# Performance work log

Hardware: AMD Instinct MI355X
Metric: run time of the kernel (lower is better)

Reference implementation:

```python
import jax, jax.numpy as jnp
import numpy as np

BS, QLEN, DIM, NH = 2, 2048, 1024, 16
HD = DIM // NH


def setup_inputs() -> dict:
    key = jax.random.key(0)
    ks = jax.random.split(key, 6)
    std = 0.02
    return {
        "x": jax.random.normal(ks[0], (BS, QLEN, DIM), dtype=jnp.float32),
        "mask": jnp.ones((BS, QLEN), dtype=jnp.float32),
        "Wq": jax.random.normal(ks[1], (DIM, DIM), dtype=jnp.float32) * std,
        "bq": jnp.zeros((DIM,), dtype=jnp.float32),
        "Wk": jax.random.normal(ks[2], (DIM, DIM), dtype=jnp.float32) * std,
        "bk": jnp.zeros((DIM,), dtype=jnp.float32),
        "Wv": jax.random.normal(ks[3], (DIM, DIM), dtype=jnp.float32) * std,
        "bv": jnp.zeros((DIM,), dtype=jnp.float32),
        "Wo": jax.random.normal(ks[4], (DIM, DIM), dtype=jnp.float32) * std,
        "bo": jnp.zeros((DIM,), dtype=jnp.float32),
    }


def reference(x, mask, Wq, bq, Wk, bk, Wv, bv, Wo, bo):
    bs, qlen, dim = x.shape
    # project and split heads: [bs, nh, len, hd]
    def split_heads(t):
        return t.reshape(bs, -1, NH, HD).transpose(0, 2, 1, 3)

    q = split_heads(x @ Wq + bq) / jnp.sqrt(jnp.float32(HD))
    k = split_heads(x @ Wk + bk)
    v = split_heads(x @ Wv + bv)

    scores = jnp.einsum("bhqd,bhkd->bhqk", q, k)  # [bs, nh, qlen, klen]
    m = mask.reshape(bs, 1, 1, -1)  # 2D mask -> broadcast over heads and q
    scores = scores - 1e30 * (1.0 - m)
    weights = jax.nn.softmax(scores, axis=-1)
    # dropout p=0.0 at inference -> no-op; head_mask is None
    context = jnp.einsum("bhqk,bhkd->bhqd", weights, v)
    context = context.transpose(0, 2, 1, 3).reshape(bs, qlen, NH * HD)
    return context @ Wo + bo
```

## Files before the change

kernel.cpp:

```cpp
#include <hip/hip_runtime.h>
#include <stdint.h>

#define BSZ  2
#define SEQ  2048
#define DIM  1024
#define NHD  16
#define HD   64
#define MTOT (BSZ*SEQ)

using short8  = __attribute__((ext_vector_type(8))) short;
using floatx4 = __attribute__((ext_vector_type(4))) float;

#define QSCALE 0.18033688011112042f
#define BIGM   1.44e30f

__device__ __forceinline__ unsigned short f2bf(float f) {
    unsigned int u = __float_as_uint(f);
    u += 0x7fffu + ((u >> 16) & 1u);
    return (unsigned short)(u >> 16);
}
__device__ __forceinline__ unsigned int pk2r(float a, float b) {
    unsigned int ua = __float_as_uint(a) + 0x8000u;
    unsigned int ub = __float_as_uint(b) + 0x8000u;
    return __builtin_amdgcn_perm(ub, ua, 0x07060302);
}
__device__ __forceinline__ unsigned int cvtpk(float a, float b) {
    unsigned int r;
    asm("v_cvt_pk_bf16_f32 %0, %1, %2" : "=v"(r) : "v"(a), "v"(b));
    return r;
}

__device__ __forceinline__ void gll16(const void* g, const void* lds) {
    unsigned int loff = (unsigned int)(unsigned long long)lds;
    __builtin_amdgcn_global_load_lds(
        (const __attribute__((address_space(1))) unsigned int*)g,
        (__attribute__((address_space(3))) unsigned int*)loff, 16, 0, 0);
}

__global__ __launch_bounds__(256)
void conv_x(const float* __restrict__ X, const float* __restrict__ mask,
            unsigned short* __restrict__ Xbf, float* __restrict__ Pen) {
    size_t i = ((size_t)blockIdx.x * 256 + threadIdx.x) * 8;
    float4 a = *(const float4*)(X + i);
    float4 b = *(const float4*)(X + i + 4);
    uint4 u = {pk2r(a.x, a.y), pk2r(a.z, a.w), pk2r(b.x, b.y), pk2r(b.z, b.w)};
    *(uint4*)(Xbf + i) = u;
    if (blockIdx.x < 2) {
        const size_t j = ((size_t)blockIdx.x * 256 + threadIdx.x) * 8;
        float4 m0 = *(const float4*)(mask + j);
        float4 m1 = *(const float4*)(mask + j + 4);
        float4 r0 = {__builtin_fmaf(m0.x, BIGM, -BIGM), __builtin_fmaf(m0.y, BIGM, -BIGM),
                     __builtin_fmaf(m0.z, BIGM, -BIGM), __builtin_fmaf(m0.w, BIGM, -BIGM)};
        float4 r1 = {__builtin_fmaf(m1.x, BIGM, -BIGM), __builtin_fmaf(m1.y, BIGM, -BIGM),
                     __builtin_fmaf(m1.z, BIGM, -BIGM), __builtin_fmaf(m1.w, BIGM, -BIGM)};
        *(float4*)(Pen + j)     = r0;
        *(float4*)(Pen + j + 4) = r1;
    }
}

__global__ __launch_bounds__(256)
void conv_wt(const float* __restrict__ Wq, const float* __restrict__ Wk,
             const float* __restrict__ Wv, const float* __restrict__ Wo,
             unsigned short* __restrict__ Wt3, unsigned short* __restrict__ Wto)
{
    __shared__ float tile[64 * 65];
    const int z = blockIdx.z;
    const float* W = (z == 0) ? Wq : (z == 1) ? Wk : (z == 2) ? Wv : Wo;
    unsigned short* out = (z < 3) ? (Wt3 + (size_t)z * DIM * DIM) : Wto;
    const int k0 = blockIdx.x * 64, n0 = blockIdx.y * 64;
    const int t = threadIdx.x;
    const int r = t >> 2, c0 = (t & 3) * 16;
#pragma unroll
    for (int j = 0; j < 4; ++j) {
        float4 v = *(const float4*)&W[(size_t)(k0 + r) * DIM + n0 + c0 + j * 4];
        tile[r * 65 + c0 + j * 4 + 0] = v.x;
        tile[r * 65 + c0 + j * 4 + 1] = v.y;
        tile[r * 65 + c0 + j * 4 + 2] = v.z;
        tile[r * 65 + c0 + j * 4 + 3] = v.w;
    }
    __syncthreads();
    unsigned int p[8];
#pragma unroll
    for (int j = 0; j < 8; ++j)
        p[j] = pk2r(tile[(c0 + 2 * j) * 65 + r], tile[(c0 + 2 * j + 1) * 65 + r]);
    uint4 u0 = {p[0], p[1], p[2], p[3]}, u1 = {p[4], p[5], p[6], p[7]};
    unsigned short* dst = out + (size_t)(n0 + r) * DIM + k0 + c0;
    *(uint4*)dst = u0;
    *(uint4*)(dst + 8) = u1;
}

__global__ __launch_bounds__(256)
void qkv_gemm(const unsigned short* __restrict__ Xbf,
              const unsigned short* __restrict__ Wt3,
              const float* __restrict__ bq, const float* __restrict__ bk,
              const float* __restrict__ bv,
              unsigned short* __restrict__ Qb,
              unsigned short* __restrict__ Kb,
              unsigned short* __restrict__ VbT)
{
    __shared__ unsigned short As[2][128 * 32];
    __shared__ unsigned short Bs[2][128 * 32];

    const int t = threadIdx.x, w = t >> 6, lane = t & 63;
    const int lm = lane & 15, grp = lane >> 4;
    const int wm = w >> 1, wn = w & 1;
    const int m0 = blockIdx.x * 128;
    const int mat = blockIdx.y >> 3;
    const int n0 = (blockIdx.y & 7) * 128;
    const unsigned short* Bg = Wt3 + (size_t)mat * DIM * DIM;
    const int lr = lane >> 2, lc = (lane & 3) * 8;
    const int r0 = w * 16;
    const bool swap = (mat != 2);

    const unsigned short* xs0 = Xbf + (size_t)(m0 + r0 + lr) * DIM + lc;
    const unsigned short* xs1 = Xbf + (size_t)(m0 + 64 + r0 + lr) * DIM + lc;
    const unsigned short* ws0 = Bg  + (size_t)(n0 + r0 + lr) * DIM + lc;
    const unsigned short* ws1 = Bg  + (size_t)(n0 + 64 + r0 + lr) * DIM + lc;

    const unsigned short* afb[2];
    const unsigned short* bfb[2];
#pragma unroll
    for (int u = 0; u < 2; ++u) {
        afb[u] = &As[u][(wm * 64 + lm) * 32 + grp * 8];
        bfb[u] = &Bs[u][(wn * 64 + lm) * 32 + grp * 8];
    }

    floatx4 acc[4][4];
#pragma unroll
    for (int i = 0; i < 4; ++i)
#pragma unroll
        for (int j = 0; j < 4; ++j) acc[i][j] = (floatx4){0.f, 0.f, 0.f, 0.f};

#define QKV_STAGE(BUF) do {                                    \
        gll16(xs0, &As[BUF][r0 * 32]);                         \
        gll16(xs1, &As[BUF][(64 + r0) * 32]);                  \
        gll16(ws0, &Bs[BUF][r0 * 32]);                         \
        gll16(ws1, &Bs[BUF][(64 + r0) * 32]);                  \
        xs0 += 32; xs1 += 32; ws0 += 32; ws1 += 32;            \
    } while (0)

#define QKV_BODY(CUR) do {                                                    \
        __syncthreads();                                                      \
        QKV_STAGE(CUR ^ 1);                                                   \
        short8 af[4], bf[4];                                                  \
        _Pragma("unroll")                                                     \
        for (int mt = 0; mt < 4; ++mt)                                        \
            af[mt] = *(const short8*)(afb[CUR] + mt * 512);                   \
        _Pragma("unroll")                                                     \
        for (int nt = 0; nt < 4; ++nt)                                        \
            bf[nt] = *(const short8*)(bfb[CUR] + nt * 512);                   \
        if (swap) {                                                           \
            _Pragma("unroll")                                                 \
            for (int mt = 0; mt < 4; ++mt)                                    \
                _Pragma("unroll")                                             \
                for (int nt = 0; nt < 4; ++nt)                                \
                    acc[mt][nt] = __builtin_amdgcn_mfma_f32_16x16x32_bf16(    \
                        bf[nt], af[mt], acc[mt][nt], 0, 0, 0);                \
        } else {                                                              \
            _Pragma("unroll")                                                 \
            for (int mt = 0; mt < 4; ++mt)                                    \
                _Pragma("unroll")                                             \
                for (int nt = 0; nt < 4; ++nt)                                \
                    acc[mt][nt] = __builtin_amdgcn_mfma_f32_16x16x32_bf16(    \
                        af[mt], bf[nt], acc[mt][nt], 0, 0, 0);                \
        }                                                                     \
    } while (0)

    QKV_STAGE(0);
#pragma unroll 1
    for (int it = 0; it < DIM / 64; ++it) {
        QKV_BODY(0);
        QKV_BODY(1);
    }
#undef QKV_BODY
#undef QKV_STAGE

    if (mat == 2) {
#pragma unroll
        for (int nt = 0; nt < 4; ++nt) {
            const int c = n0 + wn * 64 + nt * 16 + lm;
            const float bb = bv[c];
            const int h = c >> 6, d = c & 63;
#pragma unroll
            for (int mt = 0; mt < 4; ++mt) {
                const int r = m0 + wm * 64 + mt * 16 + grp * 4;
                const int b = r >> 11, s = r & 2047;
                const int si = s & 63, sb = s & ~63;
                const int cg = si >> 4, g = (si >> 2) & 3;
                const int unit = (((cg & 1) << 2) | g) ^ (d & 7);
                const int sph = sb + unit * 8 + ((cg >> 1) << 2);
                uint2 pv;
                pv.x = pk2r(acc[mt][nt][0] + bb, acc[mt][nt][1] + bb);
                pv.y = pk2r(acc[mt][nt][2] + bb, acc[mt][nt][3] + bb);
                *(uint2*)&VbT[(((size_t)(b * NHD + h)) * HD + d) * SEQ + sph] = pv;
            }
        }
    } else {
        const float* bias = (mat == 0) ? bq : bk;
        unsigned short* dst = (mat == 0) ? Qb : Kb;
        const float sc = (mat == 0) ? QSCALE : 1.0f;
#pragma unroll
        for (int nt = 0; nt < 4; ++nt) {
            const int c0 = n0 + wn * 64 + nt * 16 + grp * 4;
            float4 bb = *(const float4*)&bias[c0];
            const int h = c0 >> 6, d0 = c0 & 63;
#pragma unroll
            for (int mt = 0; mt < 4; ++mt) {
                const int r = m0 + wm * 64 + mt * 16 + lm;
                const int b = r >> 11, s = r & 2047;
                uint2 pv;
                pv.x = pk2r((acc[mt][nt][0] + bb.x) * sc, (acc[mt][nt][1] + bb.y) * sc);
                pv.y = pk2r((acc[mt][nt][2] + bb.z) * sc, (acc[mt][nt][3] + bb.w) * sc);
                const int dd = (mat == 0) ? d0
                             : ((((d0 >> 3) ^ (s & 7)) << 3) | (d0 & 7));
                *(uint2*)&dst[(((size_t)(b * NHD + h)) * SEQ + s) * HD + dd] = pv;
            }
        }
    }
}

__global__ __launch_bounds__(256, 4)
void attn(const unsigned short* __restrict__ Qb,
          const unsigned short* __restrict__ Kb,
          const unsigned short* __restrict__ VbT,
          const float* __restrict__ Pen,
          unsigned short* __restrict__ Cb)
{
    __shared__ unsigned short Kt[2][64 * 64];
    __shared__ unsigned short Vt[2][64 * 64];

    const int t = threadIdx.x, w = t >> 6, lane = t & 63;
    const int lm = lane & 15, grp = lane >> 4;
    const int x7 = lm & 7;

    const int lin = blockIdx.y * (int)gridDim.x + blockIdx.x;
    const int swz = (lin & 7) * ((SEQ / 64) * (BSZ * NHD) / 8) + (lin >> 3);
    const int bh = swz >> 5, b = bh >> 4, h = bh & 15;
    const int q0 = (swz & 31) * 64;

    short8 qf[2];
    {
        const unsigned short* qrow = Qb + ((size_t)bh * SEQ + q0 + w * 16 + lm) * HD;
        qf[0] = *(const short8*)(qrow + grp * 8);
        qf[1] = *(const short8*)(qrow + 32 + grp * 8);
    }

    const unsigned int one2 = 0x3f803f80u;
    uint4 onesu = {one2, one2, one2, one2};
    short8 ones = *(const short8*)&onesu;

    floatx4 oacc[4];
#pragma unroll
    for (int i = 0; i < 4; ++i) oacc[i] = (floatx4){0.f, 0.f, 0.f, 0.f};
    floatx4 lacc = (floatx4){0.f, 0.f, 0.f, 0.f};

    const unsigned short* Kg = Kb + (size_t)bh * SEQ * HD;
    const unsigned short* Vg = VbT + (size_t)bh * HD * SEQ;
    const int srow = lane >> 3, scol = (lane & 7) * 8;

    const unsigned short* kp0 = Kg + (size_t)(w * 16 + srow) * HD + scol;
    const unsigned short* kp1 = kp0 + 8 * HD;
    const unsigned short* vp0 = Vg + (size_t)(w * 16 + srow) * SEQ + scol;
    const unsigned short* vp1 = vp0 + 8 * SEQ;

    gll16(kp0, &Kt[0][(w * 16) * 64]);
    gll16(kp1, &Kt[0][(w * 16 + 8) * 64]);
    gll16(vp0, &Vt[0][(w * 16) * 64]);
    gll16(vp1, &Vt[0][(w * 16 + 8) * 64]);
    kp0 += 64 * HD; kp1 += 64 * HD; vp0 += 64; vp1 += 64;

    const unsigned short* kba[2]; const unsigned short* kbb[2];
    const unsigned short* vba[2]; const unsigned short* vbb[2];
#pragma unroll
    for (int u = 0; u < 2; ++u) {
        kba[u] = &Kt[u][lm * 64 + ((grp    ) ^ x7) * 8];
        kbb[u] = &Kt[u][lm * 64 + ((4 + grp) ^ x7) * 8];
        vba[u] = &Vt[u][lm * 64 + ((grp    ) ^ x7) * 8];
        vbb[u] = &Vt[u][lm * 64 + ((4 + grp) ^ x7) * 8];
    }
    const float* mp = Pen + (size_t)b * SEQ + grp * 4;

#define ATTN_BODY(CUR) do {                                                   \
        __syncthreads();                                                      \
        gll16(kp0, &Kt[CUR ^ 1][(w * 16) * 64]);                              \
        gll16(kp1, &Kt[CUR ^ 1][(w * 16 + 8) * 64]);                          \
        gll16(vp0, &Vt[CUR ^ 1][(w * 16) * 64]);                              \
        gll16(vp1, &Vt[CUR ^ 1][(w * 16 + 8) * 64]);                          \
        kp0 += 64 * HD; kp1 += 64 * HD; vp0 += 64; vp1 += 64;                 \
        float4 mdv[4];                                                        \
        _Pragma("unroll")                                                     \
        for (int cg = 0; cg < 4; ++cg)                                        \
            mdv[cg] = *(const float4*)(mp + cg * 16);                         \
        mp += 64;                                                             \
        floatx4 sv[4];                                                        \
        __builtin_amdgcn_s_setprio(1);                                        \
        _Pragma("unroll")                                                     \
        for (int cg = 0; cg < 4; ++cg) {                                      \
            short8 a0 = *(const short8*)(kba[CUR] + cg * 1024);               \
            short8 a1 = *(const short8*)(kbb[CUR] + cg * 1024);               \
            floatx4 s = (floatx4){mdv[cg].x, mdv[cg].y, mdv[cg].z, mdv[cg].w}; \
            s = __builtin_amdgcn_mfma_f32_16x16x32_bf16(a0, qf[0], s, 0, 0, 0); \
            s = __builtin_amdgcn_mfma_f32_16x16x32_bf16(a1, qf[1], s, 0, 0, 0); \
            sv[cg] = s;                                                       \
        }                                                                     \
        __builtin_amdgcn_s_setprio(0);                                        \
        short8 vf[4][2];                                                      \
        _Pragma("unroll")                                                     \
        for (int dg = 0; dg < 4; ++dg) {                                      \
            vf[dg][0] = *(const short8*)(vba[CUR] + dg * 1024);               \
            vf[dg][1] = *(const short8*)(vbb[CUR] + dg * 1024);               \
        }                                                                     \
        float p[4][4];                                                        \
        _Pragma("unroll")                                                     \
        for (int cg = 0; cg < 4; ++cg) {                                      \
            p[cg][0] = __builtin_exp2f(sv[cg][0]);                            \
            p[cg][1] = __builtin_exp2f(sv[cg][1]);                            \
            p[cg][2] = __builtin_exp2f(sv[cg][2]);                            \
            p[cg][3] = __builtin_exp2f(sv[cg][3]);                            \
        }                                                                     \
        uint4 u0, u1;                                                         \
        u0.x = cvtpk(p[0][0], p[0][1]); u0.y = cvtpk(p[0][2], p[0][3]);       \
        u0.z = cvtpk(p[2][0], p[2][1]); u0.w = cvtpk(p[2][2], p[2][3]);       \
        u1.x = cvtpk(p[1][0], p[1][1]); u1.y = cvtpk(p[1][2], p[1][3]);       \
        u1.z = cvtpk(p[3][0], p[3][1]); u1.w = cvtpk(p[3][2], p[3][3]);       \
        short8 ap0 = *(const short8*)&u0;                                     \
        short8 ap1 = *(const short8*)&u1;                                     \
        __builtin_amdgcn_s_setprio(1);                                        \
        _Pragma("unroll")                                                     \
        for (int dg = 0; dg < 4; ++dg) {                                      \
            oacc[dg] = __builtin_amdgcn_mfma_f32_16x16x32_bf16(ap0, vf[dg][0], oacc[dg], 0, 0, 0); \
            oacc[dg] = __builtin_amdgcn_mfma_f32_16x16x32_bf16(ap1, vf[dg][1], oacc[dg], 0, 0, 0); \
        }                                                                     \
        lacc = __builtin_amdgcn_mfma_f32_16x16x32_bf16(ap0, ones, lacc, 0, 0, 0); \
        lacc = __builtin_amdgcn_mfma_f32_16x16x32_bf16(ap1, ones, lacc, 0, 0, 0); \
        __builtin_amdgcn_s_setprio(0);                                        \
    } while (0)

#pragma unroll 1
    for (int it = 0; it < SEQ / 128; ++it) {
        ATTN_BODY(0);
        ATTN_BODY(1);
    }
#undef ATTN_BODY

    float inv[4];
#pragma unroll
    for (int r = 0; r < 4; ++r) inv[r] = (lacc[r] > 0.f) ? 1.0f / lacc[r] : 0.f;
#pragma unroll
    for (int dg = 0; dg < 4; ++dg)
#pragma unroll
        for (int r = 0; r < 4; ++r) {
            const int s = q0 + w * 16 + grp * 4 + r;
            Cb[((size_t)(b * SEQ + s)) * DIM + h * HD + dg * 16 + lm] =
                f2bf(oacc[dg][r] * inv[r]);
        }
}

__global__ __launch_bounds__(256)
void out_gemm(const unsigned short* __restrict__ Cb,
              const unsigned short* __restrict__ Wto,
              const float* __restrict__ bo,
              float* __restrict__ out)
{
    __shared__ unsigned short As[2][128 * 32];
    __shared__ unsigned short Bs[2][64 * 32];

    const int t = threadIdx.x, w = t >> 6, lane = t & 63;
    const int lm = lane & 15, grp = lane >> 4;
    const int m0 = blockIdx.x * 128;
    const int n0 = blockIdx.y * 64;
    const int lr = lane >> 2, lc = (lane & 3) * 8;
    const int r0 = w * 16;

    const unsigned short* cs0 = Cb  + (size_t)(m0 + r0 + lr) * DIM + lc;
    const unsigned short* cs1 = Cb  + (size_t)(m0 + 64 + r0 + lr) * DIM + lc;
    const unsigned short* ws0 = Wto + (size_t)(n0 + r0 + lr) * DIM + lc;

    const unsigned short* afb[2];
    const unsigned short* bfb[2];
#pragma unroll
    for (int u = 0; u < 2; ++u) {
        afb[u] = &As[u][(w * 32 + lm) * 32 + grp * 8];
        bfb[u] = &Bs[u][lm * 32 + grp * 8];
    }

    floatx4 acc[2][4];
#pragma unroll
    for (int i = 0; i < 2; ++i)
#pragma unroll
        for (int j = 0; j < 4; ++j) acc[i][j] = (floatx4){0.f, 0.f, 0.f, 0.f};

#define OUT_STAGE(BUF) do {                                    \
        gll16(cs0, &As[BUF][r0 * 32]);                         \
        gll16(cs1, &As[BUF][(64 + r0) * 32]);                  \
        gll16(ws0, &Bs[BUF][r0 * 32]);                         \
        cs0 += 32; cs1 += 32; ws0 += 32;                       \
    } while (0)

#define OUT_BODY(CUR) do {                                                    \
        __syncthreads();                                                      \
        OUT_STAGE(CUR ^ 1);                                                   \
        short8 af[2], bf[4];                                                  \
        _Pragma("unroll")                                                     \
        for (int mt = 0; mt < 2; ++mt)                                        \
            af[mt] = *(const short8*)(afb[CUR] + mt * 512);                   \
        _Pragma("unroll")                                                     \
        for (int nt = 0; nt < 4; ++nt)                                        \
            bf[nt] = *(const short8*)(bfb[CUR] + nt * 512);                   \
        _Pragma("unroll")                                                     \
        for (int mt = 0; mt < 2; ++mt)                                        \
            _Pragma("unroll")                                                 \
            for (int nt = 0; nt < 4; ++nt)                                    \
                acc[mt][nt] = __builtin_amdgcn_mfma_f32_16x16x32_bf16(        \
                    bf[nt], af[mt], acc[mt][nt], 0, 0, 0);                    \
    } while (0)

    OUT_STAGE(0);
#pragma unroll 1
    for (int it = 0; it < DIM / 64; ++it) {
        OUT_BODY(0);
        OUT_BODY(1);
    }
#undef OUT_BODY
#undef OUT_STAGE

#pragma unroll
    for (int nt = 0; nt < 4; ++nt) {
        const int c0 = n0 + nt * 16 + grp * 4;
        float4 bb = *(const float4*)&bo[c0];
#pragma unroll
        for (int mt = 0; mt < 2; ++mt) {
            const int r = m0 + w * 32 + mt * 16 + lm;
            float4 o = {acc[mt][nt][0] + bb.x, acc[mt][nt][1] + bb.y,
                        acc[mt][nt][2] + bb.z, acc[mt][nt][3] + bb.w};
            *(float4*)&out[(size_t)r * DIM + c0] = o;
        }
    }
}

extern "C" void kernel_launch(void* const* d_in, const int* in_sizes, int n_in,
                              void* d_out, int out_size, void* d_ws, size_t ws_size,
                              hipStream_t stream)
{
    const float* x    = (const float*)d_in[0];
    const float* mask = (const float*)d_in[1];
    const float* Wq   = (const float*)d_in[2];
    const float* bq   = (const float*)d_in[3];
    const float* Wk   = (const float*)d_in[4];
    const float* bk   = (const float*)d_in[5];
    const float* Wv   = (const float*)d_in[6];
    const float* bv   = (const float*)d_in[7];
    const float* Wo   = (const float*)d_in[8];
    const float* bo   = (const float*)d_in[9];
    float* out = (float*)d_out;

    const size_t M1 = (size_t)DIM * DIM;
    unsigned short* Qb  = (unsigned short*)d_ws;
    unsigned short* Kb  = Qb  + 4 * M1;
    unsigned short* VbT = Kb  + 4 * M1;
    unsigned short* Cb  = VbT + 4 * M1;
    unsigned short* Xbf = Cb  + 4 * M1;
    unsigned short* Wt3 = Xbf + 4 * M1;
    unsigned short* Wto = Wt3 + 3 * M1;
    float*          Pen = (float*)(Wto + M1);

    conv_x <<<dim3((MTOT * DIM) / 2048), 256, 0, stream>>>(x, mask, Xbf, Pen);
    conv_wt<<<dim3(16, 16, 4), 256, 0, stream>>>(Wq, Wk, Wv, Wo, Wt3, Wto);
    qkv_gemm<<<dim3(MTOT / 128, 24), 256, 0, stream>>>(Xbf, Wt3, bq, bk, bv, Qb, Kb, VbT);
    attn<<<dim3(SEQ / 64, BSZ * NHD), 256, 0, stream>>>(Qb, Kb, VbT, Pen, Cb);
    out_gemm<<<dim3(MTOT / 128, DIM / 64), 256, 0, stream>>>(Cb, Wto, bo, out);
}
```

Before: 201.7 us.

## Give each attention wave two query tiles and stage mask in LDS

The attention kernel drops to 128 threads per block, and each wave now handles 32 query rows (two 16-row groups) instead of 16. Each K/V fragment read from LDS therefore feeds twice as many MFMAs, which reduces LDS traffic per unit of work. The per-batch mask penalty vector is loaded once into shared memory rather than read from global memory on every iteration. In exchange, register pressure rises, launch bounds change, fewer waves per block share each barrier, and LDS use per block grows by 8KB.

```diff
diff --git a/kernel.cpp b/kernel.cpp
--- a/kernel.cpp
+++ b/kernel.cpp
@@ -219,7 +219,7 @@
     }
 }
 
-__global__ __launch_bounds__(256, 4)
+__global__ __launch_bounds__(128, 2)
 void attn(const unsigned short* __restrict__ Qb,
           const unsigned short* __restrict__ Kb,
           const unsigned short* __restrict__ VbT,
@@ -228,6 +228,7 @@
 {
     __shared__ unsigned short Kt[2][64 * 64];
     __shared__ unsigned short Vt[2][64 * 64];
+    __shared__ float Msk[SEQ];
 
     const int t = threadIdx.x, w = t >> 6, lane = t & 63;
     const int lm = lane & 15, grp = lane >> 4;
@@ -238,36 +239,51 @@
     const int bh = swz >> 5, b = bh >> 4, h = bh & 15;
     const int q0 = (swz & 31) * 64;
 
-    short8 qf[2];
-    {
-        const unsigned short* qrow = Qb + ((size_t)bh * SEQ + q0 + w * 16 + lm) * HD;
-        qf[0] = *(const short8*)(qrow + grp * 8);
-        qf[1] = *(const short8*)(qrow + 32 + grp * 8);
+    short8 qf[2][2];
+#pragma unroll
+    for (int g = 0; g < 2; ++g) {
+        const unsigned short* qrow =
+            Qb + ((size_t)bh * SEQ + q0 + w * 32 + g * 16 + lm) * HD;
+        qf[g][0] = *(const short8*)(qrow + grp * 8);
+        qf[g][1] = *(const short8*)(qrow + 32 + grp * 8);
     }
 
     const unsigned int one2 = 0x3f803f80u;
     uint4 onesu = {one2, one2, one2, one2};
-    short8 ones = *(const short8*)&onesu;
-
-    floatx4 oacc[4];
-#pragma unroll
-    for (int i = 0; i < 4; ++i) oacc[i] = (floatx4){0.f, 0.f, 0.f, 0.f};
-    floatx4 lacc = (floatx4){0.f, 0.f, 0.f, 0.f};
+    const short8 ones = *(const short8*)&onesu;
+
+    floatx4 oacc[2][4];
+#pragma unroll
+    for (int g = 0; g < 2; ++g)
+#pragma unroll
+        for (int i = 0; i < 4; ++i) oacc[g][i] = (floatx4){0.f, 0.f, 0.f, 0.f};
+    floatx4 lacc0 = (floatx4){0.f, 0.f, 0.f, 0.f};
+    floatx4 lacc1 = (floatx4){0.f, 0.f, 0.f, 0.f};
 
     const unsigned short* Kg = Kb + (size_t)bh * SEQ * HD;
     const unsigned short* Vg = VbT + (size_t)bh * HD * SEQ;
     const int srow = lane >> 3, scol = (lane & 7) * 8;
 
-    const unsigned short* kp0 = Kg + (size_t)(w * 16 + srow) * HD + scol;
-    const unsigned short* kp1 = kp0 + 8 * HD;
-    const unsigned short* vp0 = Vg + (size_t)(w * 16 + srow) * SEQ + scol;
-    const unsigned short* vp1 = vp0 + 8 * SEQ;
-
-    gll16(kp0, &Kt[0][(w * 16) * 64]);
-    gll16(kp1, &Kt[0][(w * 16 + 8) * 64]);
-    gll16(vp0, &Vt[0][(w * 16) * 64]);
-    gll16(vp1, &Vt[0][(w * 16 + 8) * 64]);
-    kp0 += 64 * HD; kp1 += 64 * HD; vp0 += 64; vp1 += 64;
+    {
+        const float* pb = Pen + (size_t)b * SEQ;
+#pragma unroll
+        for (int j = 0; j < 4; ++j)
+            gll16(pb + (w * 4 + j) * 256 + lane * 4, &Msk[(w * 4 + j) * 256]);
+    }
+
+    const unsigned short* kp[4];
+    const unsigned short* vp[4];
+#pragma unroll
+    for (int j = 0; j < 4; ++j) {
+        kp[j] = Kg + (size_t)(w * 32 + j * 8 + srow) * HD + scol;
+        vp[j] = Vg + (size_t)(w * 32 + j * 8 + srow) * SEQ + scol;
+    }
+#pragma unroll
+    for (int j = 0; j < 4; ++j) {
+        gll16(kp[j], &Kt[0][(w * 32 + j * 8) * 64]);
+        gll16(vp[j], &Vt[0][(w * 32 + j * 8) * 64]);
+        kp[j] += 64 * HD; vp[j] += 64;
+    }
 
     const unsigned short* kba[2]; const unsigned short* kbb[2];
     const unsigned short* vba[2]; const unsigned short* vbb[2];
@@ -278,30 +294,32 @@
         vba[u] = &Vt[u][lm * 64 + ((grp    ) ^ x7) * 8];
         vbb[u] = &Vt[u][lm * 64 + ((4 + grp) ^ x7) * 8];
     }
-    const float* mp = Pen + (size_t)b * SEQ + grp * 4;
+    const float* mp = &Msk[grp * 4];
 
 #define ATTN_BODY(CUR) do {                                                   \
         __syncthreads();                                                      \
-        gll16(kp0, &Kt[CUR ^ 1][(w * 16) * 64]);                              \
-        gll16(kp1, &Kt[CUR ^ 1][(w * 16 + 8) * 64]);                          \
-        gll16(vp0, &Vt[CUR ^ 1][(w * 16) * 64]);                              \
-        gll16(vp1, &Vt[CUR ^ 1][(w * 16 + 8) * 64]);                          \
-        kp0 += 64 * HD; kp1 += 64 * HD; vp0 += 64; vp1 += 64;                 \
+        _Pragma("unroll")                                                     \
+        for (int j = 0; j < 4; ++j) {                                         \
+            gll16(kp[j], &Kt[CUR ^ 1][(w * 32 + j * 8) * 64]);                \
+            gll16(vp[j], &Vt[CUR ^ 1][(w * 32 + j * 8) * 64]);                \
+            kp[j] += 64 * HD; vp[j] += 64;                                    \
+        }                                                                     \
         float4 mdv[4];                                                        \
         _Pragma("unroll")                                                     \
         for (int cg = 0; cg < 4; ++cg)                                        \
             mdv[cg] = *(const float4*)(mp + cg * 16);                         \
         mp += 64;                                                             \
-        floatx4 sv[4];                                                        \
+        floatx4 sv0[4], sv1[4];                                               \
         __builtin_amdgcn_s_setprio(1);                                        \
         _Pragma("unroll")                                                     \
         for (int cg = 0; cg < 4; ++cg) {                                      \
             short8 a0 = *(const short8*)(kba[CUR] + cg * 1024);               \
             short8 a1 = *(const short8*)(kbb[CUR] + cg * 1024);               \
-            floatx4 s = (floatx4){mdv[cg].x, mdv[cg].y, mdv[cg].z, mdv[cg].w}; \
-            s = __builtin_amdgcn_mfma_f32_16x16x32_bf16(a0, qf[0], s, 0, 0, 0); \
-            s = __builtin_amdgcn_mfma_f32_16x16x32_bf16(a1, qf[1], s, 0, 0, 0); \
-            sv[cg] = s;                                                       \
+            floatx4 c0 = (floatx4){mdv[cg].x, mdv[cg].y, mdv[cg].z, mdv[cg].w}; \
+            floatx4 t0 = __builtin_amdgcn_mfma_f32_16x16x32_bf16(a0, qf[0][0], c0, 0, 0, 0); \
+            sv0[cg]    = __builtin_amdgcn_mfma_f32_16x16x32_bf16(a1, qf[0][1], t0, 0, 0, 0); \
+            floatx4 t1 = __builtin_amdgcn_mfma_f32_16x16x32_bf16(a0, qf[1][0], c0, 0, 0, 0); \
+            sv1[cg]    = __builtin_amdgcn_mfma_f32_16x16x32_bf16(a1, qf[1][1], t1, 0, 0, 0); \
         }                                                                     \
         __builtin_amdgcn_s_setprio(0);                                        \
         short8 vf[4][2];                                                      \
@@ -310,29 +328,43 @@
             vf[dg][0] = *(const short8*)(vba[CUR] + dg * 1024);               \
             vf[dg][1] = *(const short8*)(vbb[CUR] + dg * 1024);               \
         }                                                                     \
-        float p[4][4];                                                        \
+        float p0[4][4], p1[4][4];                                             \
         _Pragma("unroll")                                                     \
         for (int cg = 0; cg < 4; ++cg) {                                      \
-            p[cg][0] = __builtin_exp2f(sv[cg][0]);                            \
-            p[cg][1] = __builtin_exp2f(sv[cg][1]);                            \
-            p[cg][2] = __builtin_exp2f(sv[cg][2]);                            \
-            p[cg][3] = __builtin_exp2f(sv[cg][3]);                            \
+            p0[cg][0] = __builtin_exp2f(sv0[cg][0]);                          \
+            p0[cg][1] = __builtin_exp2f(sv0[cg][1]);                          \
+            p0[cg][2] = __builtin_exp2f(sv0[cg][2]);                          \
+            p0[cg][3] = __builtin_exp2f(sv0[cg][3]);                          \
+            p1[cg][0] = __builtin_exp2f(sv1[cg][0]);                          \
+            p1[cg][1] = __builtin_exp2f(sv1[cg][1]);                          \
+            p1[cg][2] = __builtin_exp2f(sv1[cg][2]);                          \
+            p1[cg][3] = __builtin_exp2f(sv1[cg][3]);                          \
         }                                                                     \
-        uint4 u0, u1;                                                         \
-        u0.x = cvtpk(p[0][0], p[0][1]); u0.y = cvtpk(p[0][2], p[0][3]);       \
-        u0.z = cvtpk(p[2][0], p[2][1]); u0.w = cvtpk(p[2][2], p[2][3]);       \
-        u1.x = cvtpk(p[1][0], p[1][1]); u1.y = cvtpk(p[1][2], p[1][3]);       \
-        u1.z = cvtpk(p[3][0], p[3][1]); u1.w = cvtpk(p[3][2], p[3][3]);       \
-        short8 ap0 = *(const short8*)&u0;                                     \
-        short8 ap1 = *(const short8*)&u1;                                     \
+        uint4 pu0, pu1, pu2, pu3;                                             \
+        pu0.x = cvtpk(p0[0][0], p0[0][1]); pu0.y = cvtpk(p0[0][2], p0[0][3]); \
+        pu0.z = cvtpk(p0[2][0], p0[2][1]); pu0.w = cvtpk(p0[2][2], p0[2][3]); \
+        pu1.x = cvtpk(p0[1][0], p0[1][1]); pu1.y = cvtpk(p0[1][2], p0[1][3]); \
+        pu1.z = cvtpk(p0[3][0], p0[3][1]); pu1.w = cvtpk(p0[3][2], p0[3][3]); \
+        pu2.x = cvtpk(p1[0][0], p1[0][1]); pu2.y = cvtpk(p1[0][2], p1[0][3]); \
+        pu2.z = cvtpk(p1[2][0], p1[2][1]); pu2.w = cvtpk(p1[2][2], p1[2][3]); \
+        pu3.x = cvtpk(p1[1][0], p1[1][1]); pu3.y = cvtpk(p1[1][2], p1[1][3]); \
+        pu3.z = cvtpk(p1[3][0], p1[3][1]); pu3.w = cvtpk(p1[3][2], p1[3][3]); \
+        short8 ap00 = *(const short8*)&pu0;                                   \
+        short8 ap01 = *(const short8*)&pu1;                                   \
+        short8 ap10 = *(const short8*)&pu2;                                   \
+        short8 ap11 = *(const short8*)&pu3;                                   \
         __builtin_amdgcn_s_setprio(1);                                        \
         _Pragma("unroll")                                                     \
         for (int dg = 0; dg < 4; ++dg) {                                      \
-            oacc[dg] = __builtin_amdgcn_mfma_f32_16x16x32_bf16(ap0, vf[dg][0], oacc[dg], 0, 0, 0); \
-            oacc[dg] = __builtin_amdgcn_mfma_f32_16x16x32_bf16(ap1, vf[dg][1], oacc[dg], 0, 0, 0); \
+            oacc[0][dg] = __builtin_amdgcn_mfma_f32_16x16x32_bf16(ap00, vf[dg][0], oacc[0][dg], 0, 0, 0); \
+            oacc[0][dg] = __builtin_amdgcn_mfma_f32_16x16x32_bf16(ap01, vf[dg][1], oacc[0][dg], 0, 0, 0); \
+            oacc[1][dg] = __builtin_amdgcn_mfma_f32_16x16x32_bf16(ap10, vf[dg][0], oacc[1][dg], 0, 0, 0); \
+            oacc[1][dg] = __builtin_amdgcn_mfma_f32_16x16x32_bf16(ap11, vf[dg][1], oacc[1][dg], 0, 0, 0); \
         }                                                                     \
-        lacc = __builtin_amdgcn_mfma_f32_16x16x32_bf16(ap0, ones, lacc, 0, 0, 0); \
-        lacc = __builtin_amdgcn_mfma_f32_16x16x32_bf16(ap1, ones, lacc, 0, 0, 0); \
+        lacc0 = __builtin_amdgcn_mfma_f32_16x16x32_bf16(ap00, ones, lacc0, 0, 0, 0); \
+        lacc0 = __builtin_amdgcn_mfma_f32_16x16x32_bf16(ap01, ones, lacc0, 0, 0, 0); \
+        lacc1 = __builtin_amdgcn_mfma_f32_16x16x32_bf16(ap10, ones, lacc1, 0, 0, 0); \
+        lacc1 = __builtin_amdgcn_mfma_f32_16x16x32_bf16(ap11, ones, lacc1, 0, 0, 0); \
         __builtin_amdgcn_s_setprio(0);                                        \
     } while (0)
 
@@ -343,16 +375,22 @@
     }
 #undef ATTN_BODY
 
-    float inv[4];
-#pragma unroll
-    for (int r = 0; r < 4; ++r) inv[r] = (lacc[r] > 0.f) ? 1.0f / lacc[r] : 0.f;
+    float inv0[4], inv1[4];
+#pragma unroll
+    for (int r = 0; r < 4; ++r) {
+        inv0[r] = (lacc0[r] > 0.f) ? 1.0f / lacc0[r] : 0.f;
+        inv1[r] = (lacc1[r] > 0.f) ? 1.0f / lacc1[r] : 0.f;
+    }
 #pragma unroll
     for (int dg = 0; dg < 4; ++dg)
 #pragma unroll
         for (int r = 0; r < 4; ++r) {
-            const int s = q0 + w * 16 + grp * 4 + r;
-            Cb[((size_t)(b * SEQ + s)) * DIM + h * HD + dg * 16 + lm] =
-                f2bf(oacc[dg][r] * inv[r]);
+            const int s0v = q0 + w * 32 + grp * 4 + r;
+            Cb[((size_t)(b * SEQ + s0v)) * DIM + h * HD + dg * 16 + lm] =
+                f2bf(oacc[0][dg][r] * inv0[r]);
+            const int s1v = s0v + 16;
+            Cb[((size_t)(b * SEQ + s1v)) * DIM + h * HD + dg * 16 + lm] =
+                f2bf(oacc[1][dg][r] * inv1[r]);
         }
 }
 
@@ -467,6 +505,6 @@
     conv_x <<<dim3((MTOT * DIM) / 2048), 256, 0, stream>>>(x, mask, Xbf, Pen);
     conv_wt<<<dim3(16, 16, 4), 256, 0, stream>>>(Wq, Wk, Wv, Wo, Wt3, Wto);
     qkv_gemm<<<dim3(MTOT / 128, 24), 256, 0, stream>>>(Xbf, Wt3, bq, bk, bv, Qb, Kb, VbT);
-    attn<<<dim3(SEQ / 64, BSZ * NHD), 256, 0, stream>>>(Qb, Kb, VbT, Pen, Cb);
+    attn<<<dim3(SEQ / 64, BSZ * NHD), 128, 0, stream>>>(Qb, Kb, VbT, Pen, Cb);
     out_gemm<<<dim3(MTOT / 128, DIM / 64), 256, 0, stream>>>(Cb, Wto, bo, out);
 }
```

New measurement: 209.4 us. 1.04x slower.

## Split attention warps over query and key halves, merge partials via shared memory

Applied to the files above, without the earlier changes.

Each wave in the attention kernel now handles 32 query rows and half of every 64-key tile, where before it handled 16 query rows against the full tile. Every K/V fragment read from shared memory then feeds two query groups, which halves LDS fragment traffic per MFMA. The two key-half partial outputs and row sums are combined at the end through shared memory that reuses the K/V buffers. This costs extra synchronisation, a shared-memory reduction epilogue and more accumulator registers, which may lower occupancy.

```diff
diff --git a/kernel.cpp b/kernel.cpp
--- a/kernel.cpp
+++ b/kernel.cpp
@@ -226,33 +226,42 @@
           const float* __restrict__ Pen,
           unsigned short* __restrict__ Cb)
 {
-    __shared__ unsigned short Kt[2][64 * 64];
-    __shared__ unsigned short Vt[2][64 * 64];
+    __shared__ __align__(16) char smem[32768];
+    unsigned short (*Kt)[4096] = (unsigned short (*)[4096])smem;
+    unsigned short (*Vt)[4096] = (unsigned short (*)[4096])(smem + 16384);
+    float* Ep = (float*)smem;
 
     const int t = threadIdx.x, w = t >> 6, lane = t & 63;
     const int lm = lane & 15, grp = lane >> 4;
     const int x7 = lm & 7;
+    const int qh = w >> 1, kh = w & 1;
 
     const int lin = blockIdx.y * (int)gridDim.x + blockIdx.x;
     const int swz = (lin & 7) * ((SEQ / 64) * (BSZ * NHD) / 8) + (lin >> 3);
     const int bh = swz >> 5, b = bh >> 4, h = bh & 15;
     const int q0 = (swz & 31) * 64;
 
-    short8 qf[2];
-    {
-        const unsigned short* qrow = Qb + ((size_t)bh * SEQ + q0 + w * 16 + lm) * HD;
-        qf[0] = *(const short8*)(qrow + grp * 8);
-        qf[1] = *(const short8*)(qrow + 32 + grp * 8);
+    short8 qf[2][2];
+#pragma unroll
+    for (int qg = 0; qg < 2; ++qg) {
+        const unsigned short* qrow =
+            Qb + ((size_t)bh * SEQ + q0 + qh * 32 + qg * 16 + lm) * HD;
+        qf[qg][0] = *(const short8*)(qrow + grp * 8);
+        qf[qg][1] = *(const short8*)(qrow + 32 + grp * 8);
     }
 
     const unsigned int one2 = 0x3f803f80u;
     uint4 onesu = {one2, one2, one2, one2};
-    short8 ones = *(const short8*)&onesu;
-
-    floatx4 oacc[4];
-#pragma unroll
-    for (int i = 0; i < 4; ++i) oacc[i] = (floatx4){0.f, 0.f, 0.f, 0.f};
-    floatx4 lacc = (floatx4){0.f, 0.f, 0.f, 0.f};
+    const short8 ones = *(const short8*)&onesu;
+
+    floatx4 oacc[2][4];
+#pragma unroll
+    for (int qg = 0; qg < 2; ++qg)
+#pragma unroll
+        for (int i = 0; i < 4; ++i) oacc[qg][i] = (floatx4){0.f, 0.f, 0.f, 0.f};
+    floatx4 lacc[2];
+    lacc[0] = (floatx4){0.f, 0.f, 0.f, 0.f};
+    lacc[1] = (floatx4){0.f, 0.f, 0.f, 0.f};
 
     const unsigned short* Kg = Kb + (size_t)bh * SEQ * HD;
     const unsigned short* Vg = VbT + (size_t)bh * HD * SEQ;
@@ -270,69 +279,69 @@
     kp0 += 64 * HD; kp1 += 64 * HD; vp0 += 64; vp1 += 64;
 
     const unsigned short* kba[2]; const unsigned short* kbb[2];
-    const unsigned short* vba[2]; const unsigned short* vbb[2];
+    const unsigned short* vbs[2];
 #pragma unroll
     for (int u = 0; u < 2; ++u) {
-        kba[u] = &Kt[u][lm * 64 + ((grp    ) ^ x7) * 8];
-        kbb[u] = &Kt[u][lm * 64 + ((4 + grp) ^ x7) * 8];
-        vba[u] = &Vt[u][lm * 64 + ((grp    ) ^ x7) * 8];
-        vbb[u] = &Vt[u][lm * 64 + ((4 + grp) ^ x7) * 8];
-    }
-    const float* mp = Pen + (size_t)b * SEQ + grp * 4;
+        kba[u] = &Kt[u][lm * 64 + ((grp    ) ^ x7) * 8 + kh * 1024];
+        kbb[u] = &Kt[u][lm * 64 + ((4 + grp) ^ x7) * 8 + kh * 1024];
+        vbs[u] = &Vt[u][lm * 64 + (((kh ? 4 : 0) + grp) ^ x7) * 8];
+    }
+    const float* mp = Pen + (size_t)b * SEQ + kh * 16 + grp * 4;
 
 #define ATTN_BODY(CUR) do {                                                   \
         __syncthreads();                                                      \
+        float4 mdv[2];                                                        \
+        mdv[0] = *(const float4*)(mp);                                        \
+        mdv[1] = *(const float4*)(mp + 32);                                   \
+        mp += 64;                                                             \
+        __builtin_amdgcn_sched_barrier(0);                                    \
         gll16(kp0, &Kt[CUR ^ 1][(w * 16) * 64]);                              \
         gll16(kp1, &Kt[CUR ^ 1][(w * 16 + 8) * 64]);                          \
         gll16(vp0, &Vt[CUR ^ 1][(w * 16) * 64]);                              \
         gll16(vp1, &Vt[CUR ^ 1][(w * 16 + 8) * 64]);                          \
         kp0 += 64 * HD; kp1 += 64 * HD; vp0 += 64; vp1 += 64;                 \
-        float4 mdv[4];                                                        \
-        _Pragma("unroll")                                                     \
-        for (int cg = 0; cg < 4; ++cg)                                        \
-            mdv[cg] = *(const float4*)(mp + cg * 16);                         \
-        mp += 64;                                                             \
-        floatx4 sv[4];                                                        \
+        floatx4 sv[2][2];                                                     \
         __builtin_amdgcn_s_setprio(1);                                        \
         _Pragma("unroll")                                                     \
-        for (int cg = 0; cg < 4; ++cg) {                                      \
-            short8 a0 = *(const short8*)(kba[CUR] + cg * 1024);               \
-            short8 a1 = *(const short8*)(kbb[CUR] + cg * 1024);               \
-            floatx4 s = (floatx4){mdv[cg].x, mdv[cg].y, mdv[cg].z, mdv[cg].w}; \
-            s = __builtin_amdgcn_mfma_f32_16x16x32_bf16(a0, qf[0], s, 0, 0, 0); \
-            s = __builtin_amdgcn_mfma_f32_16x16x32_bf16(a1, qf[1], s, 0, 0, 0); \
-            sv[cg] = s;                                                       \
+        for (int ci = 0; ci < 2; ++ci) {                                      \
+            short8 a0 = *(const short8*)(kba[CUR] + ci * 2048);               \
+            short8 a1 = *(const short8*)(kbb[CUR] + ci * 2048);               \
+            floatx4 c0 = (floatx4){mdv[ci].x, mdv[ci].y, mdv[ci].z, mdv[ci].w}; \
+            floatx4 t0 = __builtin_amdgcn_mfma_f32_16x16x32_bf16(a0, qf[0][0], c0, 0, 0, 0); \
+            sv[0][ci]  = __builtin_amdgcn_mfma_f32_16x16x32_bf16(a1, qf[0][1], t0, 0, 0, 0); \
+            floatx4 t1 = __builtin_amdgcn_mfma_f32_16x16x32_bf16(a0, qf[1][0], c0, 0, 0, 0); \
+            sv[1][ci]  = __builtin_amdgcn_mfma_f32_16x16x32_bf16(a1, qf[1][1], t1, 0, 0, 0); \
         }                                                                     \
         __builtin_amdgcn_s_setprio(0);                                        \
-        short8 vf[4][2];                                                      \
+        short8 vf[4];                                                         \
+        _Pragma("unroll")                                                     \
+        for (int dg = 0; dg < 4; ++dg)                                        \
+            vf[dg] = *(const short8*)(vbs[CUR] + dg * 1024);                  \
+        float p[2][2][4];                                                     \
+        _Pragma("unroll")                                                     \
+        for (int qg = 0; qg < 2; ++qg)                                        \
+            _Pragma("unroll")                                                 \
+            for (int ci = 0; ci < 2; ++ci) {                                  \
+                p[qg][ci][0] = __builtin_exp2f(sv[qg][ci][0]);                \
+                p[qg][ci][1] = __builtin_exp2f(sv[qg][ci][1]);                \
+                p[qg][ci][2] = __builtin_exp2f(sv[qg][ci][2]);                \
+                p[qg][ci][3] = __builtin_exp2f(sv[qg][ci][3]);                \
+            }                                                                 \
+        uint4 pu0, pu1;                                                       \
+        pu0.x = cvtpk(p[0][0][0], p[0][0][1]); pu0.y = cvtpk(p[0][0][2], p[0][0][3]); \
+        pu0.z = cvtpk(p[0][1][0], p[0][1][1]); pu0.w = cvtpk(p[0][1][2], p[0][1][3]); \
+        pu1.x = cvtpk(p[1][0][0], p[1][0][1]); pu1.y = cvtpk(p[1][0][2], p[1][0][3]); \
+        pu1.z = cvtpk(p[1][1][0], p[1][1][1]); pu1.w = cvtpk(p[1][1][2], p[1][1][3]); \
+        short8 ap0 = *(const short8*)&pu0;                                    \
+        short8 ap1 = *(const short8*)&pu1;                                    \
+        __builtin_amdgcn_s_setprio(1);                                        \
         _Pragma("unroll")                                                     \
         for (int dg = 0; dg < 4; ++dg) {                                      \
-            vf[dg][0] = *(const short8*)(vba[CUR] + dg * 1024);               \
-            vf[dg][1] = *(const short8*)(vbb[CUR] + dg * 1024);               \
+            oacc[0][dg] = __builtin_amdgcn_mfma_f32_16x16x32_bf16(ap0, vf[dg], oacc[0][dg], 0, 0, 0); \
+            oacc[1][dg] = __builtin_amdgcn_mfma_f32_16x16x32_bf16(ap1, vf[dg], oacc[1][dg], 0, 0, 0); \
         }                                                                     \
-        float p[4][4];                                                        \
-        _Pragma("unroll")                                                     \
-        for (int cg = 0; cg < 4; ++cg) {                                      \
-            p[cg][0] = __builtin_exp2f(sv[cg][0]);                            \
-            p[cg][1] = __builtin_exp2f(sv[cg][1]);                            \
-            p[cg][2] = __builtin_exp2f(sv[cg][2]);                            \
-            p[cg][3] = __builtin_exp2f(sv[cg][3]);                            \
-        }                                                                     \
-        uint4 u0, u1;                                                         \
-        u0.x = cvtpk(p[0][0], p[0][1]); u0.y = cvtpk(p[0][2], p[0][3]);       \
-        u0.z = cvtpk(p[2][0], p[2][1]); u0.w = cvtpk(p[2][2], p[2][3]);       \
-        u1.x = cvtpk(p[1][0], p[1][1]); u1.y = cvtpk(p[1][2], p[1][3]);       \
-        u1.z = cvtpk(p[3][0], p[3][1]); u1.w = cvtpk(p[3][2], p[3][3]);       \
-        short8 ap0 = *(const short8*)&u0;                                     \
-        short8 ap1 = *(const short8*)&u1;                                     \
-        __builtin_amdgcn_s_setprio(1);                                        \
-        _Pragma("unroll")                                                     \
-        for (int dg = 0; dg < 4; ++dg) {                                      \
-            oacc[dg] = __builtin_amdgcn_mfma_f32_16x16x32_bf16(ap0, vf[dg][0], oacc[dg], 0, 0, 0); \
-            oacc[dg] = __builtin_amdgcn_mfma_f32_16x16x32_bf16(ap1, vf[dg][1], oacc[dg], 0, 0, 0); \
-        }                                                                     \
-        lacc = __builtin_amdgcn_mfma_f32_16x16x32_bf16(ap0, ones, lacc, 0, 0, 0); \
-        lacc = __builtin_amdgcn_mfma_f32_16x16x32_bf16(ap1, ones, lacc, 0, 0, 0); \
+        lacc[0] = __builtin_amdgcn_mfma_f32_16x16x32_bf16(ap0, ones, lacc[0], 0, 0, 0); \
+        lacc[1] = __builtin_amdgcn_mfma_f32_16x16x32_bf16(ap1, ones, lacc[1], 0, 0, 0); \
         __builtin_amdgcn_s_setprio(0);                                        \
     } while (0)
 
@@ -343,17 +352,46 @@
     }
 #undef ATTN_BODY
 
-    float inv[4];
-#pragma unroll
-    for (int r = 0; r < 4; ++r) inv[r] = (lacc[r] > 0.f) ? 1.0f / lacc[r] : 0.f;
-#pragma unroll
-    for (int dg = 0; dg < 4; ++dg)
-#pragma unroll
-        for (int r = 0; r < 4; ++r) {
-            const int s = q0 + w * 16 + grp * 4 + r;
-            Cb[((size_t)(b * SEQ + s)) * DIM + h * HD + dg * 16 + lm] =
-                f2bf(oacc[dg][r] * inv[r]);
+    __syncthreads();
+    if (kh) {
+        float* Eo = Ep + qh * 2048;
+        float* El = Ep + 4096 + qh * 512;
+#pragma unroll
+        for (int qg = 0; qg < 2; ++qg) {
+#pragma unroll
+            for (int dg = 0; dg < 4; ++dg)
+#pragma unroll
+                for (int r = 0; r < 4; ++r)
+                    Eo[((qg * 4 + dg) * 16 + grp * 4 + r) * 16 + lm] = oacc[qg][dg][r];
+#pragma unroll
+            for (int r = 0; r < 4; ++r)
+                El[(qg * 16 + grp * 4 + r) * 16 + lm] = lacc[qg][r];
         }
+    }
+    __syncthreads();
+    if (!kh) {
+        float* Eo = Ep + qh * 2048;
+        float* El = Ep + 4096 + qh * 512;
+#pragma unroll
+        for (int qg = 0; qg < 2; ++qg) {
+            float inv[4];
+#pragma unroll
+            for (int r = 0; r < 4; ++r) {
+                const float lt = lacc[qg][r] + El[(qg * 16 + grp * 4 + r) * 16 + lm];
+                inv[r] = (lt > 0.f) ? 1.0f / lt : 0.f;
+            }
+#pragma unroll
+            for (int dg = 0; dg < 4; ++dg)
+#pragma unroll
+                for (int r = 0; r < 4; ++r) {
+                    const float o = oacc[qg][dg][r] +
+                        Eo[((qg * 4 + dg) * 16 + grp * 4 + r) * 16 + lm];
+                    const int s = q0 + qh * 32 + qg * 16 + grp * 4 + r;
+                    Cb[((size_t)(b * SEQ + s)) * DIM + h * HD + dg * 16 + lm] =
+                        f2bf(o * inv[r]);
+                }
+        }
+    }
 }
 
 __global__ __launch_bounds__(256)
```

Result: no change. 200.2 us (-0.7%).

## Load K fragments directly from global and stage mask penalty in LDS

Applied to the files above, without the earlier changes.

The attention kernel stops staging K tiles through LDS and instead loads K fragments straight from global memory into registers each iteration, relying on the pre-swizzled K layout. The mask penalty is now computed per block into a shared array rather than by conv_x into a global buffer. The s_setprio hints around the MFMA sections are removed. This cuts LDS traffic and one buffer, but puts global-load latency for K directly on the critical path without prefetching, and every block repeats the mask conversion.

```diff
diff --git a/kernel.cpp b/kernel.cpp
--- a/kernel.cpp
+++ b/kernel.cpp
@@ -38,24 +38,12 @@
 }
 
 __global__ __launch_bounds__(256)
-void conv_x(const float* __restrict__ X, const float* __restrict__ mask,
-            unsigned short* __restrict__ Xbf, float* __restrict__ Pen) {
+void conv_x(const float* __restrict__ X, unsigned short* __restrict__ Xbf) {
     size_t i = ((size_t)blockIdx.x * 256 + threadIdx.x) * 8;
     float4 a = *(const float4*)(X + i);
     float4 b = *(const float4*)(X + i + 4);
     uint4 u = {pk2r(a.x, a.y), pk2r(a.z, a.w), pk2r(b.x, b.y), pk2r(b.z, b.w)};
     *(uint4*)(Xbf + i) = u;
-    if (blockIdx.x < 2) {
-        const size_t j = ((size_t)blockIdx.x * 256 + threadIdx.x) * 8;
-        float4 m0 = *(const float4*)(mask + j);
-        float4 m1 = *(const float4*)(mask + j + 4);
-        float4 r0 = {__builtin_fmaf(m0.x, BIGM, -BIGM), __builtin_fmaf(m0.y, BIGM, -BIGM),
-                     __builtin_fmaf(m0.z, BIGM, -BIGM), __builtin_fmaf(m0.w, BIGM, -BIGM)};
-        float4 r1 = {__builtin_fmaf(m1.x, BIGM, -BIGM), __builtin_fmaf(m1.y, BIGM, -BIGM),
-                     __builtin_fmaf(m1.z, BIGM, -BIGM), __builtin_fmaf(m1.w, BIGM, -BIGM)};
-        *(float4*)(Pen + j)     = r0;
-        *(float4*)(Pen + j + 4) = r1;
-    }
 }
 
 __global__ __launch_bounds__(256)
@@ -223,11 +211,11 @@
 void attn(const unsigned short* __restrict__ Qb,
           const unsigned short* __restrict__ Kb,
           const unsigned short* __restrict__ VbT,
-          const float* __restrict__ Pen,
+          const float* __restrict__ mask,
           unsigned short* __restrict__ Cb)
 {
-    __shared__ unsigned short Kt[2][64 * 64];
     __shared__ unsigned short Vt[2][64 * 64];
+    __shared__ float Msk[SEQ];
 
     const int t = threadIdx.x, w = t >> 6, lane = t & 63;
     const int lm = lane & 15, grp = lane >> 4;
@@ -247,7 +235,7 @@
 
     const unsigned int one2 = 0x3f803f80u;
     uint4 onesu = {one2, one2, one2, one2};
-    short8 ones = *(const short8*)&onesu;
+    const short8 ones = *(const short8*)&onesu;
 
     floatx4 oacc[4];
 #pragma unroll
@@ -258,52 +246,62 @@
     const unsigned short* Vg = VbT + (size_t)bh * HD * SEQ;
     const int srow = lane >> 3, scol = (lane & 7) * 8;
 
-    const unsigned short* kp0 = Kg + (size_t)(w * 16 + srow) * HD + scol;
-    const unsigned short* kp1 = kp0 + 8 * HD;
+    {
+        const float* mb = mask + b * SEQ;
+        const int i = t * 8;
+        float4 a = *(const float4*)(mb + i);
+        float4 c = *(const float4*)(mb + i + 4);
+        float4 ra = {__builtin_fmaf(a.x, BIGM, -BIGM), __builtin_fmaf(a.y, BIGM, -BIGM),
+                     __builtin_fmaf(a.z, BIGM, -BIGM), __builtin_fmaf(a.w, BIGM, -BIGM)};
+        float4 rc = {__builtin_fmaf(c.x, BIGM, -BIGM), __builtin_fmaf(c.y, BIGM, -BIGM),
+                     __builtin_fmaf(c.z, BIGM, -BIGM), __builtin_fmaf(c.w, BIGM, -BIGM)};
+        *(float4*)&Msk[i]     = ra;
+        *(float4*)&Msk[i + 4] = rc;
+    }
+
     const unsigned short* vp0 = Vg + (size_t)(w * 16 + srow) * SEQ + scol;
     const unsigned short* vp1 = vp0 + 8 * SEQ;
 
-    gll16(kp0, &Kt[0][(w * 16) * 64]);
-    gll16(kp1, &Kt[0][(w * 16 + 8) * 64]);
     gll16(vp0, &Vt[0][(w * 16) * 64]);
     gll16(vp1, &Vt[0][(w * 16 + 8) * 64]);
-    kp0 += 64 * HD; kp1 += 64 * HD; vp0 += 64; vp1 += 64;
-
-    const unsigned short* kba[2]; const unsigned short* kbb[2];
+    vp0 += 64; vp1 += 64;
+
+    const unsigned short* kg0 = Kg + lm * HD + (((grp    ) ^ x7) * 8);
+    const unsigned short* kg1 = Kg + lm * HD + (((4 + grp) ^ x7) * 8);
+
     const unsigned short* vba[2]; const unsigned short* vbb[2];
 #pragma unroll
     for (int u = 0; u < 2; ++u) {
-        kba[u] = &Kt[u][lm * 64 + ((grp    ) ^ x7) * 8];
-        kbb[u] = &Kt[u][lm * 64 + ((4 + grp) ^ x7) * 8];
         vba[u] = &Vt[u][lm * 64 + ((grp    ) ^ x7) * 8];
         vbb[u] = &Vt[u][lm * 64 + ((4 + grp) ^ x7) * 8];
     }
-    const float* mp = Pen + (size_t)b * SEQ + grp * 4;
+    const float* mp = &Msk[grp * 4];
 
 #define ATTN_BODY(CUR) do {                                                   \
         __syncthreads();                                                      \
-        gll16(kp0, &Kt[CUR ^ 1][(w * 16) * 64]);                              \
-        gll16(kp1, &Kt[CUR ^ 1][(w * 16 + 8) * 64]);                          \
+        short8 kf[8];                                                         \
+        _Pragma("unroll")                                                     \
+        for (int cg = 0; cg < 4; ++cg) {                                      \
+            kf[cg * 2    ] = *(const short8*)(kg0 + cg * 1024);               \
+            kf[cg * 2 + 1] = *(const short8*)(kg1 + cg * 1024);               \
+        }                                                                     \
+        kg0 += 64 * HD; kg1 += 64 * HD;                                       \
         gll16(vp0, &Vt[CUR ^ 1][(w * 16) * 64]);                              \
         gll16(vp1, &Vt[CUR ^ 1][(w * 16 + 8) * 64]);                          \
-        kp0 += 64 * HD; kp1 += 64 * HD; vp0 += 64; vp1 += 64;                 \
+        vp0 += 64; vp1 += 64;                                                 \
         float4 mdv[4];                                                        \
         _Pragma("unroll")                                                     \
         for (int cg = 0; cg < 4; ++cg)                                        \
             mdv[cg] = *(const float4*)(mp + cg * 16);                         \
         mp += 64;                                                             \
         floatx4 sv[4];                                                        \
-        __builtin_amdgcn_s_setprio(1);                                        \
         _Pragma("unroll")                                                     \
         for (int cg = 0; cg < 4; ++cg) {                                      \
-            short8 a0 = *(const short8*)(kba[CUR] + cg * 1024);               \
-            short8 a1 = *(const short8*)(kbb[CUR] + cg * 1024);               \
             floatx4 s = (floatx4){mdv[cg].x, mdv[cg].y, mdv[cg].z, mdv[cg].w}; \
-            s = __builtin_amdgcn_mfma_f32_16x16x32_bf16(a0, qf[0], s, 0, 0, 0); \
-            s = __builtin_amdgcn_mfma_f32_16x16x32_bf16(a1, qf[1], s, 0, 0, 0); \
+            s = __builtin_amdgcn_mfma_f32_16x16x32_bf16(kf[cg * 2], qf[0], s, 0, 0, 0); \
+            s = __builtin_amdgcn_mfma_f32_16x16x32_bf16(kf[cg * 2 + 1], qf[1], s, 0, 0, 0); \
             sv[cg] = s;                                                       \
         }                                                                     \
-        __builtin_amdgcn_s_setprio(0);                                        \
         short8 vf[4][2];                                                      \
         _Pragma("unroll")                                                     \
         for (int dg = 0; dg < 4; ++dg) {                                      \
@@ -325,7 +323,6 @@
         u1.z = cvtpk(p[3][0], p[3][1]); u1.w = cvtpk(p[3][2], p[3][3]);       \
         short8 ap0 = *(const short8*)&u0;                                     \
         short8 ap1 = *(const short8*)&u1;                                     \
-        __builtin_amdgcn_s_setprio(1);                                        \
         _Pragma("unroll")                                                     \
         for (int dg = 0; dg < 4; ++dg) {                                      \
             oacc[dg] = __builtin_amdgcn_mfma_f32_16x16x32_bf16(ap0, vf[dg][0], oacc[dg], 0, 0, 0); \
@@ -333,7 +330,6 @@
         }                                                                     \
         lacc = __builtin_amdgcn_mfma_f32_16x16x32_bf16(ap0, ones, lacc, 0, 0, 0); \
         lacc = __builtin_amdgcn_mfma_f32_16x16x32_bf16(ap1, ones, lacc, 0, 0, 0); \
-        __builtin_amdgcn_s_setprio(0);                                        \
     } while (0)
 
 #pragma unroll 1
@@ -462,11 +458,10 @@
     unsigned short* Xbf = Cb  + 4 * M1;
     unsigned short* Wt3 = Xbf + 4 * M1;
     unsigned short* Wto = Wt3 + 3 * M1;
-    float*          Pen = (float*)(Wto + M1);
-
-    conv_x <<<dim3((MTOT * DIM) / 2048), 256, 0, stream>>>(x, mask, Xbf, Pen);
+
+    conv_x <<<dim3((MTOT * DIM) / 2048), 256, 0, stream>>>(x, Xbf);
     conv_wt<<<dim3(16, 16, 4), 256, 0, stream>>>(Wq, Wk, Wv, Wo, Wt3, Wto);
     qkv_gemm<<<dim3(MTOT / 128, 24), 256, 0, stream>>>(Xbf, Wt3, bq, bk, bv, Qb, Kb, VbT);
-    attn<<<dim3(SEQ / 64, BSZ * NHD), 256, 0, stream>>>(Qb, Kb, VbT, Pen, Cb);
+    attn<<<dim3(SEQ / 64, BSZ * NHD), 256, 0, stream>>>(Qb, Kb, VbT, mask, Cb);
     out_gemm<<<dim3(MTOT / 128, DIM / 64), 256, 0, stream>>>(Cb, Wto, bo, out);
 }
```

Result: slower. 212.3 us (+5.2%).
